# Performance work log

Measured on AMD Instinct MI355X. Metric: run time of the kernel, lower is better.

The kernel has to match this reference:

```python
import jax, jax.numpy as jnp
import numpy as np
import math

B, N, IN, OUT, H = 2, 512, 64, 128, 8
D = OUT // H

def setup_inputs() -> dict:
    key = jax.random.key(0)
    ks = jax.random.split(key, 16)
    def lin(k, fan_in, fan_out):
        return jax.random.normal(k, (fan_in, fan_out), jnp.float32) / math.sqrt(fan_in)
    node_fts = jax.random.normal(ks[0], (B, N, IN), jnp.float32)
    edge_fts = jax.random.normal(ks[1], (B, N, N, IN), jnp.float32)
    graph_fts = jax.random.normal(ks[2], (B, IN), jnp.float32)
    hidden = jax.random.normal(ks[3], (B, N, IN), jnp.float32)
    adj = (jax.random.uniform(ks[4], (B, N, N)) < 0.3).astype(jnp.float32)
    adj = jnp.maximum(adj, jnp.eye(N, dtype=jnp.float32)[None])  # self-loops avoid zero rows
    return {
        'node_fts': node_fts, 'edge_fts': edge_fts, 'graph_fts': graph_fts,
        'hidden': hidden, 'adj_matrix': adj,
        'W_q': lin(ks[5], 2 * IN, OUT), 'W_k': lin(ks[6], 2 * IN, OUT),
        'W_v': lin(ks[7], 2 * IN, OUT), 'W_o': lin(ks[8], OUT, OUT),
        'We_k': lin(ks[9], IN, OUT),
        'ffn_W1': lin(ks[10], OUT, OUT), 'ffn_b1': jnp.zeros((OUT,), jnp.float32),
        'ffn_W2': lin(ks[11], OUT, OUT), 'ffn_b2': jnp.zeros((OUT,), jnp.float32),
    }

def reference(node_fts, edge_fts, graph_fts, hidden, adj_matrix,
              W_q, W_k, W_v, W_o, We_k, ffn_W1, ffn_b1, ffn_W2, ffn_b2):
    z = jnp.concatenate([node_fts, hidden], axis=-1)          # (B, N, 2*IN)
    def heads(x):
        return x.reshape(B, N, H, D).transpose(0, 2, 1, 3)    # (B, H, N, D)
    q = heads(z @ W_q)
    k = heads(z @ W_k)
    v = heads(z @ W_v)
    # per-edge keys: (B, H, N, N, D)
    edge_k = (edge_fts @ We_k).reshape(B, N, N, H, D).transpose(0, 3, 1, 2, 4)
    scores = jnp.einsum('bhid,bhjd->bhij', q, k)
    scores = scores + jnp.einsum('bhjd,bhijd->bhij', q, edge_k)
    scores = scores / math.sqrt(D)
    # adjacency-masked (unnormalized-exp) softmax, as in the source
    e = adj_matrix[:, None] * jnp.exp(scores)                 # (B, H, N, N)
    attn = e / jnp.sum(e, axis=-1, keepdims=True)
    out = jnp.einsum('bhij,bhjd->bhid', attn, v)              # (B, H, N, D)
    out = out.transpose(0, 2, 1, 3).reshape(B, N, OUT) @ W_o
    out = jax.nn.relu(out @ ffn_W1 + ffn_b1)
    out = jax.nn.relu(out @ ffn_W2 + ffn_b2)
    return out
```

## Files before the change

### kernel.cpp

```cpp
#include <hip/hip_runtime.h>


__device__ inline float guard_relu(float x) {
    if (x != x) return 0.0f;
    return fmaxf(x, 0.0f);
}

__global__ void tc30_prep(
    const float* node, const float* hidden,
    const float* Wq, const float* Wk, const float* Wv, const float* Wek,
    float* qbuf, float* kbuf, float* vbuf, float* qebuf)
{
    __shared__ float z[4][128];
    __shared__ float qs[4][128];
    const int t = threadIdx.x;
    const int r0 = blockIdx.x * 4;

    for (int kk = 0; kk < 2; ++kk) {
        int idx = t + kk * 256;
        int r = idx >> 7, c = idx & 127;
        int row = r0 + r;
        z[r][c] = (c < 64) ? node[row * 64 + c] : hidden[row * 64 + (c - 64)];
    }
    __syncthreads();

    const int o  = t & 127;
    const int rh = t >> 7;
    float aq0 = 0.f, aq1 = 0.f, ak0 = 0.f, ak1 = 0.f, av0 = 0.f, av1 = 0.f;
    for (int c = 0; c < 128; ++c) {
        float wq = Wq[c * 128 + o], wk = Wk[c * 128 + o], wv = Wv[c * 128 + o];
        float z0 = z[rh][c], z1 = z[rh + 2][c];
        aq0 = fmaf(z0, wq, aq0); aq1 = fmaf(z1, wq, aq1);
        ak0 = fmaf(z0, wk, ak0); ak1 = fmaf(z1, wk, ak1);
        av0 = fmaf(z0, wv, av0); av1 = fmaf(z1, wv, av1);
    }
    {
        int row0 = r0 + rh, row1 = r0 + rh + 2;
        qbuf[row0 * 128 + o] = aq0; qbuf[row1 * 128 + o] = aq1;
        kbuf[row0 * 128 + o] = ak0; kbuf[row1 * 128 + o] = ak1;
        vbuf[row0 * 128 + o] = av0; vbuf[row1 * 128 + o] = av1;
        qs[rh][o] = aq0; qs[rh + 2][o] = aq1;
    }
    __syncthreads();

    for (int kk = 0; kk < 2; ++kk) {
        int hc = t + kk * 256;
        int h = hc >> 6, c = hc & 63;
        for (int r = 0; r < 4; ++r) {
            float s = 0.f;
            for (int d = 0; d < 16; ++d)
                s = fmaf(qs[r][h * 16 + d], Wek[c * 128 + h * 16 + d], s);
            qebuf[((r0 + r) * 8 + h) * 64 + c] = s;
        }
    }
}

__global__ void __launch_bounds__(256, 4) tc30_attn(
    const float* edge, const float* adj,
    const float* qbuf, const float* kbuf, const float* vbuf,
    const float* qebuf, float* pacc, float* pden)
{
    __shared__ float qls[4][132];
    __shared__ float els[4][8][66];
    const int t   = threadIdx.x;
    const int bid = blockIdx.x;
    const int jq  = bid & 7;
    const int it  = (bid >> 3) & 127;
    const int b   = bid >> 10;
    const int i0  = it * 4;

    for (int kk = 0; kk < 2; ++kk) {
        int idx = t + kk * 256;
        int r = idx >> 7, c = idx & 127;
        qls[r][c] = qbuf[(size_t)(b * 512 + i0 + r) * 128 + c];
    }
    __syncthreads();

    const int g = t >> 3;
    const int l = t & 7;

    const int jl0 = g, jl1 = g + 32;
    const int j0 = jq * 64 + jl0;
    const int j1 = jq * 64 + jl1;

    const float* e00 = edge + ((size_t)(b * 512 + i0) * 512 + j0) * 64 + l * 8;
    const float* e10 = edge + ((size_t)(b * 512 + i0) * 512 + j1) * 64 + l * 8;
    float4 ea0[4], eb0[4], ea1[4], eb1[4];
    #pragma unroll
    for (int r = 0; r < 4; ++r) {
        const float* p0 = e00 + (size_t)r * 512 * 64;
        const float* p1 = e10 + (size_t)r * 512 * 64;
        ea0[r] = *(const float4*)(p0);
        eb0[r] = *(const float4*)(p0 + 4);
        ea1[r] = *(const float4*)(p1);
        eb1[r] = *(const float4*)(p1 + 4);
    }
    float am0[4], am1[4];
    #pragma unroll
    for (int r = 0; r < 4; ++r) {
        am0[r] = adj[(size_t)(b * 512 + i0 + r) * 512 + j0];
        am1[r] = adj[(size_t)(b * 512 + i0 + r) * 512 + j1];
    }
    const float* qer0 = qebuf + (size_t)(b * 512 + j0) * 512 + l * 8;
    const float* qer1 = qebuf + (size_t)(b * 512 + j1) * 512 + l * 8;
    const float* kr0  = kbuf  + (size_t)(b * 512 + j0) * 128;
    const float* kr1  = kbuf  + (size_t)(b * 512 + j1) * 128;

    #pragma unroll
    for (int h = 0; h < 8; ++h) {
        float4 qa0 = *(const float4*)(qer0 + h * 64);
        float4 qb0 = *(const float4*)(qer0 + h * 64 + 4);
        float4 qa1 = *(const float4*)(qer1 + h * 64);
        float4 qb1 = *(const float4*)(qer1 + h * 64 + 4);
        float k00 = kr0[h * 16 + l], k01 = kr0[h * 16 + 8 + l];
        float k10 = kr1[h * 16 + l], k11 = kr1[h * 16 + 8 + l];
        float p0[4], p1[4];
        #pragma unroll
        for (int r = 0; r < 4; ++r) {
            float qv  = qls[r][h * 16 + l];
            float qvb = qls[r][h * 16 + 8 + l];
            p0[r] = ea0[r].x*qa0.x + ea0[r].y*qa0.y + ea0[r].z*qa0.z + ea0[r].w*qa0.w
                  + eb0[r].x*qb0.x + eb0[r].y*qb0.y + eb0[r].z*qb0.z + eb0[r].w*qb0.w
                  + k00 * qv + k01 * qvb;
            p1[r] = ea1[r].x*qa1.x + ea1[r].y*qa1.y + ea1[r].z*qa1.z + ea1[r].w*qa1.w
                  + eb1[r].x*qb1.x + eb1[r].y*qb1.y + eb1[r].z*qb1.z + eb1[r].w*qb1.w
                  + k10 * qv + k11 * qvb;
        }
        #pragma unroll
        for (int m = 4; m >= 1; m >>= 1) {
            #pragma unroll
            for (int r = 0; r < 4; ++r) {
                p0[r] += __shfl_xor(p0[r], m, 64);
                p1[r] += __shfl_xor(p1[r], m, 64);
            }
        }
        if (l == h) {
            #pragma unroll
            for (int r = 0; r < 4; ++r) {
                els[r][h][jl0] = am0[r] * __expf(p0[r] * 0.25f);
                els[r][h][jl1] = am1[r] * __expf(p1[r] * 0.25f);
            }
        }
    }
    __syncthreads();

    const int o  = t & 127;
    const int ip = t >> 7;
    const int hB = o >> 4;
    const float* vbase = vbuf + ((size_t)(b * 512) + jq * 64) * 128 + o;
    float acc0 = 0.f, acc1 = 0.f, d0 = 0.f, d1 = 0.f;
    #pragma unroll 8
    for (int jl = 0; jl < 64; ++jl) {
        float v  = vbase[(size_t)jl * 128];
        float e0 = els[ip][hB][jl];
        float e1 = els[ip + 2][hB][jl];
        acc0 = fmaf(e0, v, acc0); d0 += e0;
        acc1 = fmaf(e1, v, acc1); d1 += e1;
    }
    size_t ix0 = ((size_t)(b * 512 + i0 + ip) * 8 + jq) * 128 + o;
    size_t ix1 = ((size_t)(b * 512 + i0 + ip + 2) * 8 + jq) * 128 + o;
    pacc[ix0] = acc0; pden[ix0] = d0;
    pacc[ix1] = acc1; pden[ix1] = d1;
}

__global__ void tc30_post(
    const float* pacc, const float* pden,
    const float* Wo, const float* W1,
    const float* b1f, const float* W2, const float* b2f,
    float* __restrict__ out)
{
    __shared__ float a[4][128];
    __shared__ float y[4][128];
    const int t = threadIdx.x;
    const int o = t & 127, rh = t >> 7;
    const int r0 = blockIdx.x * 4;

    for (int m = 0; m < 2; ++m) {
        int r = rh + 2 * m;
        int row = r0 + r;
        float s = 0.f, d = 0.f;
        #pragma unroll
        for (int q = 0; q < 8; ++q) {
            size_t idx = ((size_t)row * 8 + q) * 128 + o;
            s += pacc[idx];
            d += pden[idx];
        }
        a[r][o] = s / d;
    }
    __syncthreads();

    float acc0 = 0.f, acc1 = 0.f;
    for (int c = 0; c < 128; ++c) {
        float w = Wo[c * 128 + o];
        acc0 = fmaf(a[rh][c], w, acc0);
        acc1 = fmaf(a[rh + 2][c], w, acc1);
    }
    y[rh][o] = acc0; y[rh + 2][o] = acc1;
    __syncthreads();

    acc0 = 0.f; acc1 = 0.f;
    for (int c = 0; c < 128; ++c) {
        float w = W1[c * 128 + o];
        acc0 = fmaf(y[rh][c], w, acc0);
        acc1 = fmaf(y[rh + 2][c], w, acc1);
    }
    float bb = b1f[o];
    __syncthreads();
    a[rh][o]     = guard_relu(acc0 + bb);
    a[rh + 2][o] = guard_relu(acc1 + bb);
    __syncthreads();

    acc0 = 0.f; acc1 = 0.f;
    for (int c = 0; c < 128; ++c) {
        float w = W2[c * 128 + o];
        acc0 = fmaf(a[rh][c], w, acc0);
        acc1 = fmaf(a[rh + 2][c], w, acc1);
    }
    float bb2 = b2f[o];
    int row0 = r0 + rh, row1 = r0 + rh + 2;
    out[row0 * 128 + o] = guard_relu(acc0 + bb2);
    out[row1 * 128 + o] = guard_relu(acc1 + bb2);
}

extern "C" void kernel_launch(void* const* d_in, const int* in_sizes, int n_in,
                              void* d_out, int out_size, void* d_ws, size_t ws_size,
                              hipStream_t stream) {
    (void)in_sizes; (void)n_in; (void)out_size; (void)ws_size;

    const float* node   = (const float*)d_in[0];
    const float* edge   = (const float*)d_in[1];
    const float* hidden = (const float*)d_in[3];
    const float* adj    = (const float*)d_in[4];
    const float* Wq     = (const float*)d_in[5];
    const float* Wk     = (const float*)d_in[6];
    const float* Wv     = (const float*)d_in[7];
    const float* Wo     = (const float*)d_in[8];
    const float* Wek    = (const float*)d_in[9];
    const float* W1     = (const float*)d_in[10];
    const float* b1f    = (const float*)d_in[11];
    const float* W2     = (const float*)d_in[12];
    const float* b2f    = (const float*)d_in[13];
    float* out = (float*)d_out;

    float* ws    = (float*)d_ws;
    float* qbuf  = ws;
    float* kbuf  = qbuf  + 131072;
    float* vbuf  = kbuf  + 131072;
    float* qebuf = vbuf  + 131072;
    float* pacc  = qebuf + 524288;
    float* pden  = pacc  + 1048576;

    tc30_prep<<<256, 256, 0, stream>>>(node, hidden, Wq, Wk, Wv, Wek,
                                       qbuf, kbuf, vbuf, qebuf);
    tc30_attn<<<2048, 256, 0, stream>>>(edge, adj, qbuf, kbuf, vbuf, qebuf,
                                        pacc, pden);
    tc30_post<<<256, 256, 0, stream>>>(pacc, pden, Wo, W1, b1f, W2, b2f, out);
}
```

Baseline: 78.90 us.

## Make attention waves independent with per-wave partial sums and no block barriers

The attention kernel is restructured so each 64-lane wave owns 16 key columns and keeps its own slice of exp-weights in shared memory. This removes both __syncthreads barriers and the shared-memory staging of q, which is now read straight from global memory. Partial numerators and denominators are written per wave, so the partial buffers grow fourfold and the post kernel now reduces 32 partials per row instead of 8. The trade is less intra-block synchronisation against much more partial-sum traffic through global memory and a larger workspace requirement. The launch_bounds occupancy hint is also dropped.

```diff
diff --git a/kernel.cpp b/kernel.cpp
--- a/kernel.cpp
+++ b/kernel.cpp
@@ -6,7 +6,7 @@
     return fmaxf(x, 0.0f);
 }
 
-__global__ void tc30_prep(
+__global__ void tc31_prep(
     const float* node, const float* hidden,
     const float* Wq, const float* Wk, const float* Wv, const float* Wek,
     float* qbuf, float* kbuf, float* vbuf, float* qebuf)
@@ -55,13 +55,12 @@
     }
 }
 
-__global__ void __launch_bounds__(256, 4) tc30_attn(
+__global__ void tc31_attn(
     const float* edge, const float* adj,
     const float* qbuf, const float* kbuf, const float* vbuf,
     const float* qebuf, float* pacc, float* pden)
 {
-    __shared__ float qls[4][132];
-    __shared__ float els[4][8][66];
+    __shared__ float els[4][4][8][18];
     const int t   = threadIdx.x;
     const int bid = blockIdx.x;
     const int jq  = bid & 7;
@@ -69,19 +68,15 @@
     const int b   = bid >> 10;
     const int i0  = it * 4;
 
-    for (int kk = 0; kk < 2; ++kk) {
-        int idx = t + kk * 256;
-        int r = idx >> 7, c = idx & 127;
-        qls[r][c] = qbuf[(size_t)(b * 512 + i0 + r) * 128 + c];
-    }
-    __syncthreads();
-
-    const int g = t >> 3;
-    const int l = t & 7;
-
-    const int jl0 = g, jl1 = g + 32;
-    const int j0 = jq * 64 + jl0;
-    const int j1 = jq * 64 + jl1;
+    const int w    = t >> 6;
+    const int lane = t & 63;
+    const int g    = lane >> 3;
+    const int l    = lane & 7;
+
+    const int jbase = jq * 64 + w * 16;
+    const int jl0 = g, jl1 = g + 8;
+    const int j0 = jbase + jl0;
+    const int j1 = jbase + jl1;
 
     const float* e00 = edge + ((size_t)(b * 512 + i0) * 512 + j0) * 64 + l * 8;
     const float* e10 = edge + ((size_t)(b * 512 + i0) * 512 + j1) * 64 + l * 8;
@@ -105,6 +100,7 @@
     const float* qer1 = qebuf + (size_t)(b * 512 + j1) * 512 + l * 8;
     const float* kr0  = kbuf  + (size_t)(b * 512 + j0) * 128;
     const float* kr1  = kbuf  + (size_t)(b * 512 + j1) * 128;
+    const float* qrow = qbuf  + (size_t)(b * 512 + i0) * 128;
 
     #pragma unroll
     for (int h = 0; h < 8; ++h) {
@@ -117,8 +113,8 @@
         float p0[4], p1[4];
         #pragma unroll
         for (int r = 0; r < 4; ++r) {
-            float qv  = qls[r][h * 16 + l];
-            float qvb = qls[r][h * 16 + 8 + l];
+            float qv  = qrow[r * 128 + h * 16 + l];
+            float qvb = qrow[r * 128 + h * 16 + 8 + l];
             p0[r] = ea0[r].x*qa0.x + ea0[r].y*qa0.y + ea0[r].z*qa0.z + ea0[r].w*qa0.w
                   + eb0[r].x*qb0.x + eb0[r].y*qb0.y + eb0[r].z*qb0.z + eb0[r].w*qb0.w
                   + k00 * qv + k01 * qvb;
@@ -137,33 +133,39 @@
         if (l == h) {
             #pragma unroll
             for (int r = 0; r < 4; ++r) {
-                els[r][h][jl0] = am0[r] * __expf(p0[r] * 0.25f);
-                els[r][h][jl1] = am1[r] * __expf(p1[r] * 0.25f);
+                els[w][r][h][jl0] = am0[r] * __expf(p0[r] * 0.25f);
+                els[w][r][h][jl1] = am1[r] * __expf(p1[r] * 0.25f);
             }
         }
     }
-    __syncthreads();
-
-    const int o  = t & 127;
-    const int ip = t >> 7;
-    const int hB = o >> 4;
-    const float* vbase = vbuf + ((size_t)(b * 512) + jq * 64) * 128 + o;
-    float acc0 = 0.f, acc1 = 0.f, d0 = 0.f, d1 = 0.f;
-    #pragma unroll 8
-    for (int jl = 0; jl < 64; ++jl) {
-        float v  = vbase[(size_t)jl * 128];
-        float e0 = els[ip][hB][jl];
-        float e1 = els[ip + 2][hB][jl];
-        acc0 = fmaf(e0, v, acc0); d0 += e0;
-        acc1 = fmaf(e1, v, acc1); d1 += e1;
-    }
-    size_t ix0 = ((size_t)(b * 512 + i0 + ip) * 8 + jq) * 128 + o;
-    size_t ix1 = ((size_t)(b * 512 + i0 + ip + 2) * 8 + jq) * 128 + o;
-    pacc[ix0] = acc0; pden[ix0] = d0;
-    pacc[ix1] = acc1; pden[ix1] = d1;
-}
-
-__global__ void tc30_post(
+
+    #pragma unroll
+    for (int half = 0; half < 2; ++half) {
+        const int o  = lane + half * 64;
+        const int hB = o >> 4;
+        const float* vbase = vbuf + ((size_t)(b * 512) + jbase) * 128 + o;
+        float acc[4] = {0.f, 0.f, 0.f, 0.f};
+        float den[4] = {0.f, 0.f, 0.f, 0.f};
+        #pragma unroll 4
+        for (int jl = 0; jl < 16; ++jl) {
+            float v = vbase[(size_t)jl * 128];
+            #pragma unroll
+            for (int r = 0; r < 4; ++r) {
+                float e = els[w][r][hB][jl];
+                acc[r] = fmaf(e, v, acc[r]);
+                den[r] += e;
+            }
+        }
+        #pragma unroll
+        for (int r = 0; r < 4; ++r) {
+            size_t ix = ((size_t)(b * 512 + i0 + r) * 32 + (jq * 4 + w)) * 128 + o;
+            pacc[ix] = acc[r];
+            pden[ix] = den[r];
+        }
+    }
+}
+
+__global__ void tc31_post(
     const float* pacc, const float* pden,
     const float* Wo, const float* W1,
     const float* b1f, const float* W2, const float* b2f,
@@ -179,9 +181,9 @@
         int r = rh + 2 * m;
         int row = r0 + r;
         float s = 0.f, d = 0.f;
-        #pragma unroll
-        for (int q = 0; q < 8; ++q) {
-            size_t idx = ((size_t)row * 8 + q) * 128 + o;
+        #pragma unroll 8
+        for (int q = 0; q < 32; ++q) {
+            size_t idx = ((size_t)row * 32 + q) * 128 + o;
             s += pacc[idx];
             d += pden[idx];
         }
@@ -248,11 +250,11 @@
     float* vbuf  = kbuf  + 131072;
     float* qebuf = vbuf  + 131072;
     float* pacc  = qebuf + 524288;
-    float* pden  = pacc  + 1048576;
-
-    tc30_prep<<<256, 256, 0, stream>>>(node, hidden, Wq, Wk, Wv, Wek,
+    float* pden  = pacc  + 4194304;
+
+    tc31_prep<<<256, 256, 0, stream>>>(node, hidden, Wq, Wk, Wv, Wek,
                                        qbuf, kbuf, vbuf, qebuf);
-    tc30_attn<<<2048, 256, 0, stream>>>(edge, adj, qbuf, kbuf, vbuf, qebuf,
+    tc31_attn<<<2048, 256, 0, stream>>>(edge, adj, qbuf, kbuf, vbuf, qebuf,
                                         pacc, pden);
-    tc30_post<<<256, 256, 0, stream>>>(pacc, pden, Wo, W1, b1f, W2, b2f, out);
-}
+    tc31_post<<<256, 256, 0, stream>>>(pacc, pden, Wo, W1, b1f, W2, b2f, out);
+}
```

After: 84.34 us. 6.9% more time.
